# Performance work log

Hardware: AMD Instinct MI355X
Metric: run time of the kernel (lower is better)

Reference implementation:

```python
import jax, jax.numpy as jnp
import numpy as np

B, W, LOCAL, GLOBAL = 32, 16, 64, 64
EMB, HIDDEN, OUT, NLAYERS = 256, 512, 64, 3
T = 128  # output_len


def setup_inputs() -> dict:
    key = jax.random.key(0)
    ks = jax.random.split(key, 16)
    s = 0.05
    inp = {
        "z_t": jax.random.normal(ks[0], (B, W, LOCAL), jnp.float32),
        "z_g": jax.random.normal(ks[1], (B, GLOBAL), jnp.float32),
        # embedding: Linear(local+global -> 256, bias=False), torch layout (out,in)
        "w_emb": jax.random.normal(ks[2], (EMB, LOCAL + GLOBAL), jnp.float32) * s,
        # GRU(input_size=1, hidden=256); input is all-zeros so w_ih contributes
        # nothing (only its bias b_ih matters) -> faithfully omit w_ih.
        "gru_w_hh": jax.random.normal(ks[3], (3 * EMB, EMB), jnp.float32) * s,
        "gru_b_ih": jax.random.normal(ks[4], (3 * EMB,), jnp.float32) * s,
        "gru_b_hh": jax.random.normal(ks[5], (3 * EMB,), jnp.float32) * s,
        "mlp_w1": jax.random.normal(ks[6], (HIDDEN, EMB), jnp.float32) * s,
        "mlp_b1": jax.random.normal(ks[7], (HIDDEN,), jnp.float32) * s,
        "mlp_w2": jax.random.normal(ks[8], (HIDDEN, HIDDEN), jnp.float32) * s,
        "mlp_b2": jax.random.normal(ks[9], (HIDDEN,), jnp.float32) * s,
        "mlp_w3": jax.random.normal(ks[10], (HIDDEN, HIDDEN), jnp.float32) * s,
        "mlp_b3": jax.random.normal(ks[11], (HIDDEN,), jnp.float32) * s,
        "mu_w": jax.random.normal(ks[12], (OUT, HIDDEN), jnp.float32) * s,
        "mu_b": jax.random.normal(ks[13], (OUT,), jnp.float32) * s,
        "output_len": T,
    }
    return inp


def _gru_zero_input(h0, w_hh, b_ih, b_hh, length):
    # PyTorch GRU cell with x_t == 0: input-to-hidden term reduces to b_ih.
    b_ir, b_iz, b_in = jnp.split(b_ih, 3)

    def step(h, _):
        gh = h @ w_hh.T + b_hh              # (BW, 3*EMB)
        g_r, g_z, g_n = jnp.split(gh, 3, axis=-1)
        r = jax.nn.sigmoid(b_ir + g_r)
        z = jax.nn.sigmoid(b_iz + g_z)
        n = jnp.tanh(b_in + r * g_n)
        h_new = (1.0 - z) * n + z * h
        return h_new, h_new

    _, hs = jax.lax.scan(step, h0, None, length=length)
    return hs  # (T, BW, EMB)


def reference(z_t, z_g, w_emb, gru_w_hh, gru_b_ih, gru_b_hh,
              mlp_w1, mlp_b1, mlp_w2, mlp_b2, mlp_w3, mlp_b3,
              mu_w, mu_b, output_len):
    b, nw, _ = z_t.shape
    z = jnp.concatenate(
        [z_t, jnp.broadcast_to(z_g[:, None, :], (b, nw, z_g.shape[-1]))], axis=-1)
    emb = z @ w_emb.T                        # (B, W, EMB)
    h0 = emb.reshape(b * nw, -1)             # (BW, EMB) initial hidden state

    hs = _gru_zero_input(h0, gru_w_hh, gru_b_ih, gru_b_hh, output_len)
    h_t = jnp.transpose(hs, (1, 0, 2))       # (BW, T, EMB), batch_first

    # MLP: Linear+ELU (Dropout p=0.05 is identity in eval)
    h = jax.nn.elu(h_t @ mlp_w1.T + mlp_b1)
    h = jax.nn.elu(h @ mlp_w2.T + mlp_b2)
    h = jax.nn.elu(h @ mlp_w3.T + mlp_b3)
    x_mean = h @ mu_w.T + mu_b               # (BW, T, OUT)
    return x_mean.reshape(b, nw * output_len, -1)
```

## Files before the change

### kernel.cpp

```cpp
#include <hip/hip_runtime.h>
#include <hip/hip_bf16.h>


typedef __bf16 bf16_t;
typedef __bf16 bf16x2 __attribute__((ext_vector_type(2)));
typedef __bf16 bf16x4 __attribute__((ext_vector_type(4)));
typedef __bf16 bf16x8 __attribute__((ext_vector_type(8)));
typedef float f32x4 __attribute__((ext_vector_type(4)));

#define MFMA16(a, b, c) __builtin_amdgcn_mfma_f32_16x16x32_bf16(a, b, c, 0, 0, 0)

#define EMB 256
#define TSTEPS 128
#define OUTD 64

#define HS_OFF   0u
#define H0_OFF   33554432u
#define WHH_OFF  34078720u
#define W1_OFF   34471936u
#define W2_OFF   34734080u
#define W3_OFF   35258368u
#define MUW_OFF  35782656u

__device__ __forceinline__ float rcpf(float x){ return __builtin_amdgcn_rcpf(x); }
__device__ __forceinline__ void lds_barrier() {
  asm volatile("s_waitcnt lgkmcnt(0)\n\ts_barrier" ::: "memory");
}
__device__ __forceinline__ float eluf(float x) {
  return (x > 0.f) ? x : (__expf(x) - 1.f);
}
__device__ __forceinline__ bf16x8 cvt8(const float* __restrict__ s) {
  const float4 a = *reinterpret_cast<const float4*>(s);
  const float4 b = *reinterpret_cast<const float4*>(s + 4);
  bf16x8 v;
  v[0] = (bf16_t)a.x; v[1] = (bf16_t)a.y; v[2] = (bf16_t)a.z; v[3] = (bf16_t)a.w;
  v[4] = (bf16_t)b.x; v[5] = (bf16_t)b.y; v[6] = (bf16_t)b.z; v[7] = (bf16_t)b.w;
  return v;
}

template<int KC, int LOGKC>
__device__ __forceinline__ void conv_frag8(
    const float* __restrict__ src, bf16_t* __restrict__ dst,
    int NK8, int g, int G)
{
  const int K = KC * 128;
  for (int i8 = g; i8 < NK8; i8 += G) {
    const int l15  = i8 & 15;
    const int quad = (i8 >> 4) & 3;
    const int kk   = (i8 >> 6) & 3;
    const int rem  = i8 >> 8;
    const int kc   = rem & (KC - 1);
    const int nt   = rem >> LOGKC;
    *reinterpret_cast<bf16x8*>(dst + (size_t)i8 * 8) =
        cvt8(src + (size_t)(nt * 16 + l15) * K + kc * 128 + kk * 32 + quad * 8);
  }
}

__global__ __launch_bounds__(256) void ce_kernel(
    const float* __restrict__ z_t, const float* __restrict__ z_g,
    const float* __restrict__ w_emb, float* __restrict__ h0,
    const float* __restrict__ whh, const float* __restrict__ w1,
    const float* __restrict__ w2, const float* __restrict__ w3,
    const float* __restrict__ muw, char* __restrict__ ws)
{
  const int tid = threadIdx.x;
  if (blockIdx.x < 512) {
    __shared__ float zrow[128];
    const int bw = blockIdx.x;
    if (tid < 128)
      zrow[tid] = (tid < 64) ? z_t[bw * 64 + tid] : z_g[(bw >> 4) * 64 + (tid - 64)];
    __syncthreads();
    const float4* wp = reinterpret_cast<const float4*>(w_emb + (size_t)tid * 128);
    float s = 0.f;
#pragma unroll
    for (int k4 = 0; k4 < 32; ++k4) {
      const float4 w = wp[k4];
      s += zrow[k4 * 4 + 0] * w.x + zrow[k4 * 4 + 1] * w.y
         + zrow[k4 * 4 + 2] * w.z + zrow[k4 * 4 + 3] * w.w;
    }
    h0[(size_t)bw * 256 + tid] = s;
  } else {
    const int g = (blockIdx.x - 512) * 256 + tid;
    const int G = 256 * 256;
    bf16_t* d = (bf16_t*)(ws + WHH_OFF);
    for (int i8 = g; i8 < 24576; i8 += G)
      *reinterpret_cast<bf16x8*>(d + (size_t)i8 * 8) = cvt8(whh + (size_t)i8 * 8);
    conv_frag8<2, 1>(w1,  (bf16_t*)(ws + W1_OFF),  16384, g, G);
    conv_frag8<4, 2>(w2,  (bf16_t*)(ws + W2_OFF),  32768, g, G);
    conv_frag8<4, 2>(w3,  (bf16_t*)(ws + W3_OFF),  32768, g, G);
    conv_frag8<4, 2>(muw, (bf16_t*)(ws + MUW_OFF),  4096, g, G);
  }
}

__global__ __launch_bounds__(512, 2) void gru_kernel(
    const float* __restrict__ h0, const bf16_t* __restrict__ w_hh,
    const float* __restrict__ b_ih, const float* __restrict__ b_hh,
    bf16_t* __restrict__ hs)
{
  __shared__ __align__(16) bf16_t h16[2][16][272];

  const int tid  = threadIdx.x;
  const int wv   = tid >> 6;
  const int lane = tid & 63;
  const int l15  = lane & 15;
  const int quad = lane >> 4;
  const int bw0  = blockIdx.x * 4;
  const int cA   = wv * 32 + l15;

  bf16x8 wf[6][8];
#pragma unroll
  for (int g = 0; g < 3; ++g)
#pragma unroll
    for (int s = 0; s < 2; ++s) {
      const int n = g * 256 + cA + s * 16;
#pragma unroll
      for (int kk = 0; kk < 8; ++kk)
        wf[g * 2 + s][kk] = *reinterpret_cast<const bf16x8*>(
            w_hh + (size_t)n * 256 + kk * 32 + quad * 8);
    }

  float br[2], bz[2], bin[2], bhn[2], hm[2];
#pragma unroll
  for (int s = 0; s < 2; ++s) {
    const int c = cA + s * 16;
    br[s]  = b_ih[c]       + b_hh[c];
    bz[s]  = b_ih[256 + c] + b_hh[256 + c];
    bin[s] = b_ih[512 + c];
    bhn[s] = b_hh[512 + c];
    hm[s]  = h0[(size_t)(bw0 + quad) * 256 + c];
  }

  {
    bf16x8 zv;
#pragma unroll
    for (int e = 0; e < 8; ++e) zv[e] = (bf16_t)0.f;
    for (int i = tid; i < 1088; i += 512)
      reinterpret_cast<bf16x8*>(h16)[i] = zv;
  }
  __syncthreads();
#pragma unroll
  for (int s = 0; s < 2; ++s)
    h16[0][quad * 4][cA + s * 16] = (bf16_t)hm[s];
  __syncthreads();

  bf16_t* hsp = hs + ((size_t)(bw0 + quad) * TSTEPS) * EMB + cA;

#pragma unroll 1
  for (int t = 0; t < TSTEPS; ++t) {
    const bf16_t (*hr)[272] = h16[t & 1];
    bf16_t (*hw)[272] = h16[(t & 1) ^ 1];

    f32x4 acc[6] = {};
#pragma unroll
    for (int kk = 0; kk < 8; ++kk) {
      const bf16x8 a = *reinterpret_cast<const bf16x8*>(&hr[l15][kk * 32 + quad * 8]);
#pragma unroll
      for (int ct = 0; ct < 6; ++ct)
        acc[ct] = MFMA16(a, wf[ct][kk], acc[ct]);
    }

#pragma unroll
    for (int s = 0; s < 2; ++s) {
      const float gr = acc[s][0]     + br[s];
      const float gz = acc[2 + s][0] + bz[s];
      const float gn = acc[4 + s][0] + bhn[s];
      const float rr = rcpf(1.f + __expf(-gr));
      const float zz = rcpf(1.f + __expf(-gz));
      const float pre = bin[s] + rr * gn;
      const float nn = 1.f - 2.f * rcpf(__expf(2.f * pre) + 1.f);
      hm[s] = nn + zz * (hm[s] - nn);
      const bf16_t nh = (bf16_t)hm[s];
      hw[quad * 4][cA + s * 16] = nh;
      hsp[(size_t)t * EMB + s * 16] = nh;
    }
    lds_barrier();
  }
}

template<int KC>
__device__ __forceinline__ void mlp_layer(
    const bf16_t* __restrict__ Wf, const float* __restrict__ bias,
    bf16_t (*act)[520], int wv, int lane, int l15, int quad)
{
  constexpr int NIT = KC * 4;
  f32x4 acc[8][4] = {};
  bf16x8 wf[2][8];

#pragma unroll
  for (int ct = 0; ct < 8; ++ct)
    wf[0][ct] = *reinterpret_cast<const bf16x8*>(
        Wf + (((size_t)(wv * 8 + ct) * KC) << 11) + lane * 8);

#pragma unroll
  for (int it = 0; it < NIT; ++it) {
    const int cur = it & 1, nxt = cur ^ 1;
    if (it + 1 < NIT) {
      const int kc1 = (it + 1) >> 2, kk1 = (it + 1) & 3;
#pragma unroll
      for (int ct = 0; ct < 8; ++ct)
        wf[nxt][ct] = *reinterpret_cast<const bf16x8*>(
            Wf + ((((size_t)(wv * 8 + ct) * KC + kc1) * 4 + kk1) << 9) + lane * 8);
    }
    const int kc = it >> 2, kk = it & 3;
    bf16x8 a8[4];
#pragma unroll
    for (int mt = 0; mt < 4; ++mt)
      a8[mt] = *reinterpret_cast<const bf16x8*>(
          &act[mt * 16 + l15][kc * 128 + kk * 32 + quad * 8]);
#pragma unroll
    for (int mt = 0; mt < 4; ++mt)
#pragma unroll
      for (int ct = 0; ct < 8; ++ct)
        acc[ct][mt] = MFMA16(wf[cur][ct], a8[mt], acc[ct][mt]);
  }

  __syncthreads();
#pragma unroll
  for (int ct = 0; ct < 8; ++ct) {
    const int nb = (wv * 8 + ct) * 16 + quad * 4;
    const float4 b4 = *reinterpret_cast<const float4*>(bias + nb);
#pragma unroll
    for (int mt = 0; mt < 4; ++mt) {
      bf16x4 v;
      v[0] = (bf16_t)eluf(acc[ct][mt][0] + b4.x);
      v[1] = (bf16_t)eluf(acc[ct][mt][1] + b4.y);
      v[2] = (bf16_t)eluf(acc[ct][mt][2] + b4.z);
      v[3] = (bf16_t)eluf(acc[ct][mt][3] + b4.w);
      *reinterpret_cast<bf16x4*>(&act[mt * 16 + l15][nb]) = v;
    }
  }
  __syncthreads();
}

__global__ __launch_bounds__(256, 2) void mlp_kernel(
    const bf16_t* __restrict__ hs,
    const bf16_t* __restrict__ w1, const float* __restrict__ b1,
    const bf16_t* __restrict__ w2, const float* __restrict__ b2,
    const bf16_t* __restrict__ w3, const float* __restrict__ b3,
    const bf16_t* __restrict__ muw, const float* __restrict__ mub,
    float* __restrict__ out)
{
  __shared__ __align__(16) bf16_t act[64][520];

  const int tid  = threadIdx.x;
  const int wv   = tid >> 6;
  const int lane = tid & 63;
  const int l15  = lane & 15;
  const int quad = lane >> 4;
  const size_t r0 = (size_t)blockIdx.x * 64;

  for (int v = tid; v < 64 * 32; v += 256) {
    const int rr = v >> 5, cc = v & 31;
    bf16x8 x = *reinterpret_cast<const bf16x8*>(hs + (r0 + rr) * EMB + cc * 8);
    *reinterpret_cast<bf16x8*>(&act[rr][cc * 8]) = x;
  }
  __syncthreads();

  mlp_layer<2>(w1, b1, act, wv, lane, l15, quad);
  mlp_layer<4>(w2, b2, act, wv, lane, l15, quad);
  mlp_layer<4>(w3, b3, act, wv, lane, l15, quad);

  f32x4 macc[4] = {};
  const int n = wv * 16 + l15;
#pragma unroll
  for (int it = 0; it < 16; ++it) {
    const int kc = it >> 2, kk = it & 3;
    bf16x8 wfm = *reinterpret_cast<const bf16x8*>(
        muw + ((((size_t)wv * 4 + kc) * 4 + kk) << 9) + lane * 8);
#pragma unroll
    for (int i = 0; i < 4; ++i) {
      bf16x8 a = *reinterpret_cast<const bf16x8*>(
          &act[i * 16 + l15][kc * 128 + kk * 32 + quad * 8]);
      macc[i] = MFMA16(a, wfm, macc[i]);
    }
  }
  const float mb = mub[n];
#pragma unroll
  for (int i = 0; i < 4; ++i)
#pragma unroll
    for (int r = 0; r < 4; ++r)
      out[(r0 + i * 16 + quad * 4 + r) * OUTD + n] = macc[i][r] + mb;
}

extern "C" void kernel_launch(void* const* d_in, const int* in_sizes, int n_in,
                              void* d_out, int out_size, void* d_ws, size_t ws_size,
                              hipStream_t stream) {
  char* ws = (char*)d_ws;

  ce_kernel<<<768, 256, 0, stream>>>(
      (const float*)d_in[0], (const float*)d_in[1], (const float*)d_in[2],
      (float*)(ws + H0_OFF),
      (const float*)d_in[3], (const float*)d_in[6], (const float*)d_in[8],
      (const float*)d_in[10], (const float*)d_in[12], ws);

  gru_kernel<<<128, 512, 0, stream>>>(
      (const float*)(ws + H0_OFF), (const bf16_t*)(ws + WHH_OFF),
      (const float*)d_in[4], (const float*)d_in[5],
      (bf16_t*)(ws + HS_OFF));

  mlp_kernel<<<1024, 256, 0, stream>>>(
      (const bf16_t*)(ws + HS_OFF),
      (const bf16_t*)(ws + W1_OFF), (const float*)d_in[7],
      (const bf16_t*)(ws + W2_OFF), (const float*)d_in[9],
      (const bf16_t*)(ws + W3_OFF), (const float*)d_in[11],
      (const bf16_t*)(ws + MUW_OFF), (const float*)d_in[13],
      (float*)d_out);
}
```

Before: 322.7 us.

## Fuse embedding and weight conversion into GRU kernel, swizzle hidden-state LDS

Removes the separate conversion/embedding kernel: each GRU block now computes its own four initial hidden states from z_t/z_g and w_emb, converts w_hh from fp32 directly into register fragments, and also converts the MLP weights into their bf16 fragment layout in the workspace. The hidden-state LDS buffer switches from padded rows to an XOR-swizzled layout to avoid bank conflicts. This saves one launch and a global round trip for h0 and w_hh. The cost is extra prologue work on only 128 blocks, so it runs at lower parallelism than the 768-block kernel it replaces.

```diff
diff --git a/kernel.cpp b/kernel.cpp
--- a/kernel.cpp
+++ b/kernel.cpp
@@ -15,8 +15,6 @@
 #define OUTD 64
 
 #define HS_OFF   0u
-#define H0_OFF   33554432u
-#define WHH_OFF  34078720u
 #define W1_OFF   34471936u
 #define W2_OFF   34734080u
 #define W3_OFF   35258368u
@@ -56,48 +54,18 @@
   }
 }
 
-__global__ __launch_bounds__(256) void ce_kernel(
+__global__ __launch_bounds__(512, 2) void gru_kernel(
     const float* __restrict__ z_t, const float* __restrict__ z_g,
-    const float* __restrict__ w_emb, float* __restrict__ h0,
-    const float* __restrict__ whh, const float* __restrict__ w1,
-    const float* __restrict__ w2, const float* __restrict__ w3,
-    const float* __restrict__ muw, char* __restrict__ ws)
+    const float* __restrict__ w_emb,
+    const float* __restrict__ w_hh,
+    const float* __restrict__ b_ih, const float* __restrict__ b_hh,
+    const float* __restrict__ w1s, const float* __restrict__ w2s,
+    const float* __restrict__ w3s, const float* __restrict__ muws,
+    char* __restrict__ ws, bf16_t* __restrict__ hs)
 {
-  const int tid = threadIdx.x;
-  if (blockIdx.x < 512) {
-    __shared__ float zrow[128];
-    const int bw = blockIdx.x;
-    if (tid < 128)
-      zrow[tid] = (tid < 64) ? z_t[bw * 64 + tid] : z_g[(bw >> 4) * 64 + (tid - 64)];
-    __syncthreads();
-    const float4* wp = reinterpret_cast<const float4*>(w_emb + (size_t)tid * 128);
-    float s = 0.f;
-#pragma unroll
-    for (int k4 = 0; k4 < 32; ++k4) {
-      const float4 w = wp[k4];
-      s += zrow[k4 * 4 + 0] * w.x + zrow[k4 * 4 + 1] * w.y
-         + zrow[k4 * 4 + 2] * w.z + zrow[k4 * 4 + 3] * w.w;
-    }
-    h0[(size_t)bw * 256 + tid] = s;
-  } else {
-    const int g = (blockIdx.x - 512) * 256 + tid;
-    const int G = 256 * 256;
-    bf16_t* d = (bf16_t*)(ws + WHH_OFF);
-    for (int i8 = g; i8 < 24576; i8 += G)
-      *reinterpret_cast<bf16x8*>(d + (size_t)i8 * 8) = cvt8(whh + (size_t)i8 * 8);
-    conv_frag8<2, 1>(w1,  (bf16_t*)(ws + W1_OFF),  16384, g, G);
-    conv_frag8<4, 2>(w2,  (bf16_t*)(ws + W2_OFF),  32768, g, G);
-    conv_frag8<4, 2>(w3,  (bf16_t*)(ws + W3_OFF),  32768, g, G);
-    conv_frag8<4, 2>(muw, (bf16_t*)(ws + MUW_OFF),  4096, g, G);
-  }
-}
-
-__global__ __launch_bounds__(512, 2) void gru_kernel(
-    const float* __restrict__ h0, const bf16_t* __restrict__ w_hh,
-    const float* __restrict__ b_ih, const float* __restrict__ b_hh,
-    bf16_t* __restrict__ hs)
-{
-  __shared__ __align__(16) bf16_t h16[2][16][272];
+  __shared__ __align__(16) char  h16raw[2 * 16 * 544];
+  __shared__ __align__(16) float zrow[4][128];
+  __shared__ __align__(16) float h0s[4][256];
 
   const int tid  = threadIdx.x;
   const int wv   = tid >> 6;
@@ -107,6 +75,44 @@
   const int bw0  = blockIdx.x * 4;
   const int cA   = wv * 32 + l15;
 
+  if (tid < 512) {
+    const int row = tid >> 7, k = tid & 127;
+    zrow[row][k] = (k < 64) ? z_t[(bw0 + row) * 64 + k]
+                            : z_g[((bw0 + row) >> 4) * 64 + (k - 64)];
+  }
+  {
+    bf16x8 zv;
+#pragma unroll
+    for (int e = 0; e < 8; ++e) zv[e] = (bf16_t)0.f;
+    for (int i = tid; i < 1088; i += 512)
+      reinterpret_cast<bf16x8*>(h16raw)[i] = zv;
+  }
+  __syncthreads();
+
+  {
+    const int r = tid >> 8, c = tid & 255;
+    const float4* wp = reinterpret_cast<const float4*>(w_emb + (size_t)c * 128);
+    float s0 = 0.f, s1 = 0.f;
+#pragma unroll
+    for (int k4 = 0; k4 < 32; ++k4) {
+      const float4 w = wp[k4];
+      s0 += zrow[r][k4*4+0]*w.x + zrow[r][k4*4+1]*w.y
+          + zrow[r][k4*4+2]*w.z + zrow[r][k4*4+3]*w.w;
+      s1 += zrow[r+2][k4*4+0]*w.x + zrow[r+2][k4*4+1]*w.y
+          + zrow[r+2][k4*4+2]*w.z + zrow[r+2][k4*4+3]*w.w;
+    }
+    h0s[r][c] = s0;
+    h0s[r+2][c] = s1;
+  }
+  {
+    const int g = blockIdx.x * 512 + tid;
+    const int G = 128 * 512;
+    conv_frag8<2, 1>(w1s,  (bf16_t*)(ws + W1_OFF),  16384, g, G);
+    conv_frag8<4, 2>(w2s,  (bf16_t*)(ws + W2_OFF),  32768, g, G);
+    conv_frag8<4, 2>(w3s,  (bf16_t*)(ws + W3_OFF),  32768, g, G);
+    conv_frag8<4, 2>(muws, (bf16_t*)(ws + MUW_OFF),  4096, g, G);
+  }
+
   bf16x8 wf[6][8];
 #pragma unroll
   for (int g = 0; g < 3; ++g)
@@ -115,8 +121,7 @@
       const int n = g * 256 + cA + s * 16;
 #pragma unroll
       for (int kk = 0; kk < 8; ++kk)
-        wf[g * 2 + s][kk] = *reinterpret_cast<const bf16x8*>(
-            w_hh + (size_t)n * 256 + kk * 32 + quad * 8);
+        wf[g * 2 + s][kk] = cvt8(w_hh + (size_t)n * 256 + kk * 32 + quad * 8);
     }
 
   float br[2], bz[2], bin[2], bhn[2], hm[2];
@@ -127,33 +132,37 @@
     bz[s]  = b_ih[256 + c] + b_hh[256 + c];
     bin[s] = b_ih[512 + c];
     bhn[s] = b_hh[512 + c];
-    hm[s]  = h0[(size_t)(bw0 + quad) * 256 + c];
-  }
-
-  {
-    bf16x8 zv;
-#pragma unroll
-    for (int e = 0; e < 8; ++e) zv[e] = (bf16_t)0.f;
-    for (int i = tid; i < 1088; i += 512)
-      reinterpret_cast<bf16x8*>(h16)[i] = zv;
-  }
-  __syncthreads();
-#pragma unroll
-  for (int s = 0; s < 2; ++s)
-    h16[0][quad * 4][cA + s * 16] = (bf16_t)hm[s];
+  }
+  __syncthreads();
+
+#pragma unroll
+  for (int s = 0; s < 2; ++s) {
+    hm[s] = h0s[quad][cA + s * 16];
+    const int row = quad * 4;
+    const int col2 = (cA + s * 16) * 2;
+    *reinterpret_cast<bf16_t*>(
+        h16raw + row * 544 + (col2 ^ ((row & 7) << 4))) = (bf16_t)hm[s];
+  }
   __syncthreads();
 
   bf16_t* hsp = hs + ((size_t)(bw0 + quad) * TSTEPS) * EMB + cA;
+
+  const int rd_base = l15 * 544;
+  const int rd_swz  = (l15 & 7) << 4;
+  const int wr_row  = quad * 4;
+  const int wr_swz  = (wr_row & 7) << 4;
 
 #pragma unroll 1
   for (int t = 0; t < TSTEPS; ++t) {
-    const bf16_t (*hr)[272] = h16[t & 1];
-    bf16_t (*hw)[272] = h16[(t & 1) ^ 1];
+    const char* hr = h16raw + (t & 1) * 8704;
+    char*       hw = h16raw + (((t & 1) ^ 1)) * 8704;
 
     f32x4 acc[6] = {};
 #pragma unroll
     for (int kk = 0; kk < 8; ++kk) {
-      const bf16x8 a = *reinterpret_cast<const bf16x8*>(&hr[l15][kk * 32 + quad * 8]);
+      const int col2 = (kk * 32 + quad * 8) * 2;
+      const bf16x8 a = *reinterpret_cast<const bf16x8*>(
+          hr + rd_base + (col2 ^ rd_swz));
 #pragma unroll
       for (int ct = 0; ct < 6; ++ct)
         acc[ct] = MFMA16(a, wf[ct][kk], acc[ct]);
@@ -170,7 +179,8 @@
       const float nn = 1.f - 2.f * rcpf(__expf(2.f * pre) + 1.f);
       hm[s] = nn + zz * (hm[s] - nn);
       const bf16_t nh = (bf16_t)hm[s];
-      hw[quad * 4][cA + s * 16] = nh;
+      const int col2 = (cA + s * 16) * 2;
+      *reinterpret_cast<bf16_t*>(hw + wr_row * 544 + (col2 ^ wr_swz)) = nh;
       hsp[(size_t)t * EMB + s * 16] = nh;
     }
     lds_barrier();
@@ -287,16 +297,12 @@
                               hipStream_t stream) {
   char* ws = (char*)d_ws;
 
-  ce_kernel<<<768, 256, 0, stream>>>(
+  gru_kernel<<<128, 512, 0, stream>>>(
       (const float*)d_in[0], (const float*)d_in[1], (const float*)d_in[2],
-      (float*)(ws + H0_OFF),
-      (const float*)d_in[3], (const float*)d_in[6], (const float*)d_in[8],
-      (const float*)d_in[10], (const float*)d_in[12], ws);
-
-  gru_kernel<<<128, 512, 0, stream>>>(
-      (const float*)(ws + H0_OFF), (const bf16_t*)(ws + WHH_OFF),
-      (const float*)d_in[4], (const float*)d_in[5],
-      (bf16_t*)(ws + HS_OFF));
+      (const float*)d_in[3], (const float*)d_in[4], (const float*)d_in[5],
+      (const float*)d_in[6], (const float*)d_in[8], (const float*)d_in[10],
+      (const float*)d_in[12],
+      ws, (bf16_t*)(ws + HS_OFF));
 
   mlp_kernel<<<1024, 256, 0, stream>>>(
       (const bf16_t*)(ws + HS_OFF),
```

Measured after the change: 355.6 us. +10.2%, slower.
